# Performance work log

Hardware: AMD Instinct MI355X
Metric: run time of the kernel (lower is better)

The kernel has to match this reference:

```python
import jax, jax.numpy as jnp
import numpy as np
import math

LEVEL_SHAPES = [(100, 152), (50, 76), (25, 38), (13, 19)]
BS, E, NH, NL, NP = 2, 256, 8, 4, 4


def _grid_init_bias(num_heads, num_levels, num_points):
    # faithful to MultiScaleDeformableAttention.init_weights sampling_offsets bias
    thetas = jnp.arange(num_heads, dtype=jnp.float32) * (2.0 * math.pi / num_heads)
    grid = jnp.stack([jnp.cos(thetas), jnp.sin(thetas)], -1)  # [H,2]
    grid = grid / jnp.max(jnp.abs(grid), axis=-1, keepdims=True)
    grid = jnp.tile(grid[:, None, None, :], (1, num_levels, num_points, 1))  # [H,L,P,2]
    scale = jnp.arange(1, num_points + 1, dtype=jnp.float32)[None, None, :, None]
    return (grid * scale).reshape(-1)


def setup_inputs() -> dict:
    key = jax.random.key(0)
    ks = jax.random.split(key, 10)
    nv = sum(h * w for h, w in LEVEL_SHAPES)  # 20197
    nq = nv
    query = jax.random.normal(ks[0], (BS, nq, E), dtype=jnp.float32)
    value = jax.random.normal(ks[1], (BS, nv, E), dtype=jnp.float32)
    reference_points = jax.random.uniform(ks[2], (BS, nq, NL, 2), dtype=jnp.float32)
    spatial_shapes = jnp.array(LEVEL_SHAPES, dtype=jnp.int32)
    sizes = [h * w for h, w in LEVEL_SHAPES]
    level_start_index = jnp.array(np.cumsum([0] + sizes)[:-1], dtype=jnp.int32)
    s = 1.0 / math.sqrt(E)
    # Linear params stored as [in, out]; y = x @ W + b
    Wv = jax.random.normal(ks[3], (E, E), dtype=jnp.float32) * s
    bv = jnp.zeros((E,), jnp.float32)
    Wso = jax.random.normal(ks[4], (E, NH * NL * NP * 2), dtype=jnp.float32) * 0.01
    bso = _grid_init_bias(NH, NL, NP)
    Waw = jax.random.normal(ks[5], (E, NH * NL * NP), dtype=jnp.float32) * 0.01
    baw = jnp.zeros((NH * NL * NP,), jnp.float32)
    Wo = jax.random.normal(ks[6], (E, E), dtype=jnp.float32) * s
    bo = jnp.zeros((E,), jnp.float32)
    return dict(query=query, value=value, reference_points=reference_points,
                spatial_shapes=spatial_shapes, level_start_index=level_start_index,
                Wv=Wv, bv=bv, Wso=Wso, bso=bso, Waw=Waw, baw=baw, Wo=Wo, bo=bo)


def _bilinear_sample(vl, loc, h, w):
    # vl: [bs, nh, h*w, d]; loc: [bs, nq, nh, P, 2] normalized in [0,1]
    # matches F.grid_sample(mode='bilinear', padding_mode='zeros', align_corners=False)
    bs, nh, _, d = vl.shape
    nq, P = loc.shape[1], loc.shape[3]
    x = loc[..., 0] * w - 0.5
    y = loc[..., 1] * h - 0.5
    x0 = jnp.floor(x).astype(jnp.int32); x1 = x0 + 1
    y0 = jnp.floor(y).astype(jnp.int32); y1 = y0 + 1
    wx1 = x - x0; wx0 = 1.0 - wx1
    wy1 = y - y0; wy0 = 1.0 - wy1

    def gather(ix, iy):
        valid = ((ix >= 0) & (ix < w) & (iy >= 0) & (iy < h)).astype(vl.dtype)
        idx = jnp.clip(iy, 0, h - 1) * w + jnp.clip(ix, 0, w - 1)  # [bs,nq,nh,P]
        idx = jnp.transpose(idx, (0, 2, 1, 3)).reshape(bs, nh, nq * P)
        g = jnp.take_along_axis(vl, idx[..., None], axis=2)  # [bs,nh,nq*P,d]
        g = g.reshape(bs, nh, nq, P, d).transpose(0, 2, 1, 3, 4)  # [bs,nq,nh,P,d]
        return g * valid[..., None]

    return (gather(x0, y0) * (wx0 * wy0)[..., None]
            + gather(x1, y0) * (wx1 * wy0)[..., None]
            + gather(x0, y1) * (wx0 * wy1)[..., None]
            + gather(x1, y1) * (wx1 * wy1)[..., None])


def reference(query, value, reference_points, spatial_shapes, level_start_index,
              Wv, bv, Wso, bso, Waw, baw, Wo, bo):
    bs, nq, e = query.shape
    nv = value.shape[1]
    nh, nl, npt = NH, NL, NP
    d = e // nh
    shapes = np.asarray(spatial_shapes)          # static level shapes
    starts = np.asarray(level_start_index)

    v = (value @ Wv + bv).reshape(bs, nv, nh, d).transpose(0, 2, 1, 3)  # [bs,nh,nv,d]
    so = (query @ Wso + bso).reshape(bs, nq, nh, nl, npt, 2)
    aw = jax.nn.softmax((query @ Waw + baw).reshape(bs, nq, nh, nl * npt), axis=-1)
    aw = aw.reshape(bs, nq, nh, nl, npt)

    # offset normalizer is (w, h) per level
    offset_norm = jnp.stack([spatial_shapes[:, 1], spatial_shapes[:, 0]], -1).astype(query.dtype)
    loc = reference_points[:, :, None, :, None, :] + so / offset_norm[None, None, None, :, None, :]

    out = jnp.zeros((bs, nq, nh, d), dtype=query.dtype)
    for l in range(nl):
        h, w = int(shapes[l, 0]), int(shapes[l, 1])
        s = int(starts[l])
        vl = v[:, :, s:s + h * w, :]                      # [bs,nh,h*w,d]
        sampled = _bilinear_sample(vl, loc[:, :, :, l], h, w)  # [bs,nq,nh,P,d]
        out = out + jnp.einsum('bqhpd,bqhp->bqhd', sampled, aw[:, :, :, l])

    out = out.reshape(bs, nq, e) @ Wo + bo
    return out + query  # identity residual (dropout in eval mode)
```

## Files before the change

kernel.cpp:

```cpp
#include <hip/hip_runtime.h>
#include <hip/hip_bf16.h>
#include <math.h>

constexpr int kBS = 2;
constexpr int kNQ = 20197;
constexpr int kNV = 20197;
constexpr int kM  = kBS * kNQ;
constexpr int kMpad = 40448;

__constant__ int cLH[4] = {100, 50, 25, 13};
__constant__ int cLW[4] = {152, 76, 38, 19};
__constant__ int cLS[4] = {0, 15200, 19000, 19950};

typedef __bf16 bf16x8 __attribute__((ext_vector_type(8)));
typedef float  f32x4  __attribute__((ext_vector_type(4)));

__device__ __forceinline__ unsigned short f2bf(float x) {
    unsigned u = __float_as_uint(x);
    return (unsigned short)((u + 0x7fffu + ((u >> 16) & 1u)) >> 16);
}
__device__ __forceinline__ unsigned pack2(float a, float b) {
    return (unsigned)f2bf(a) | ((unsigned)f2bf(b) << 16);
}
__device__ __forceinline__ float bflo(unsigned u) { return __uint_as_float(u << 16); }
__device__ __forceinline__ float bfhi(unsigned u) { return __uint_as_float(u & 0xffff0000u); }
__device__ __forceinline__ void gload_lds16(const void* g, void* s) {
    __builtin_amdgcn_global_load_lds(
        (const __attribute__((address_space(1))) void*)g,
        (__attribute__((address_space(3))) void*)s, 16, 0, 0);
}

__global__ __launch_bounds__(256) void prep(
    const float* __restrict__ Wv, const float* __restrict__ Wso,
    const float* __restrict__ Waw, const float* __restrict__ Wo,
    const float* __restrict__ bso, const float* __restrict__ baw,
    unsigned short* __restrict__ WvT, unsigned short* __restrict__ WsoawT,
    unsigned short* __restrict__ WoT, float* __restrict__ bias384)
{
    int i = blockIdx.x * 256 + threadIdx.x;
    if (i < 65536) { int n = i >> 8, k = i & 255; WvT[i] = f2bf(Wv[k * 256 + n]); return; }
    i -= 65536;
    if (i < 98304) {
        int n = i >> 8, k = i & 255;
        WsoawT[i] = f2bf(n < 256 ? Wso[k * 256 + n] : Waw[k * 128 + (n - 256)]);
        return;
    }
    i -= 98304;
    if (i < 65536) { int n = i >> 8, k = i & 255; WoT[i] = f2bf(Wo[k * 256 + n]); return; }
    i -= 65536;
    if (i < 384) bias384[i] = (i < 256) ? bso[i] : baw[i - 256];
}

__global__ __launch_bounds__(256) void gemm_dual(
    const float* __restrict__ A0, const __hip_bfloat16* __restrict__ BT0,
    const float* __restrict__ bias0, unsigned short* __restrict__ C0,
    const float* __restrict__ A1, const __hip_bfloat16* __restrict__ BT1,
    const float* __restrict__ bias1, unsigned short* __restrict__ C1)
{
    constexpr int APITCH = 40;
    __shared__ __hip_bfloat16 As[128 * APITCH];
    __shared__ __hip_bfloat16 Bs[128 * 32];

    const int bx = blockIdx.x;
    const bool second = bx >= 2;
    const float* A = second ? A1 : A0;
    const __hip_bfloat16* BT = second ? BT1 : BT0;
    const float* bias = second ? bias1 : bias0;
    unsigned short* C = second ? C1 : C0;
    const int N = second ? 384 : 256;
    const int n0 = (second ? bx - 2 : bx) * 128;
    const int m0 = blockIdx.y * 128;

    const int t = threadIdx.x;
    const int wave = t >> 6, lane = t & 63;
    const int quad = lane >> 4, l16 = lane & 15;
    const int mw = (wave & 1) * 64, nw = (wave >> 1) * 64;
    const int sm = t >> 1;
    const int sh = (t & 1) * 16;

    f32x4 acc[4][4] = {};

    for (int k0 = 0; k0 < 256; k0 += 32) {
        __syncthreads();
        {
            const char* bt = (const char*)BT;
            #pragma unroll
            for (int j = 0; j < 2; ++j) {
                int off = j * 4096 + t * 16;
                int row = off >> 6, kb = off & 63;
                gload_lds16(bt + (size_t)(n0 + row) * 512 + k0 * 2 + kb,
                            (char*)Bs + off);
            }
        }
        {
            float4 f0 = make_float4(0.f, 0.f, 0.f, 0.f), f1 = f0, f2 = f0, f3 = f0;
            if (m0 + sm < kM) {
                const float4* p = (const float4*)(A + (size_t)(m0 + sm) * 256 + k0 + sh);
                f0 = p[0]; f1 = p[1]; f2 = p[2]; f3 = p[3];
            }
            uint4 q0 = make_uint4(pack2(f0.x, f0.y), pack2(f0.z, f0.w),
                                  pack2(f1.x, f1.y), pack2(f1.z, f1.w));
            uint4 q1 = make_uint4(pack2(f2.x, f2.y), pack2(f2.z, f2.w),
                                  pack2(f3.x, f3.y), pack2(f3.z, f3.w));
            uint4* dst = (uint4*)(void*)&As[sm * APITCH + sh];
            dst[0] = q0; dst[1] = q1;
        }
        __syncthreads();
        bf16x8 afr[4], bfr[4];
        #pragma unroll
        for (int mt = 0; mt < 4; ++mt)
            afr[mt] = *(const bf16x8*)(const void*)&As[(mw + mt * 16 + l16) * APITCH + quad * 8];
        #pragma unroll
        for (int nt = 0; nt < 4; ++nt)
            bfr[nt] = *(const bf16x8*)(const void*)&Bs[(nw + nt * 16 + l16) * 32 + quad * 8];
        #pragma unroll
        for (int mt = 0; mt < 4; ++mt)
            #pragma unroll
            for (int nt = 0; nt < 4; ++nt)
                acc[mt][nt] = __builtin_amdgcn_mfma_f32_16x16x32_bf16(
                    afr[mt], bfr[nt], acc[mt][nt], 0, 0, 0);
    }

    #pragma unroll
    for (int nt = 0; nt < 4; ++nt) {
        int col = n0 + nw + nt * 16 + l16;
        float bvv = bias[col];
        #pragma unroll
        for (int mt = 0; mt < 4; ++mt) {
            #pragma unroll
            for (int i = 0; i < 4; ++i) {
                int row = m0 + mw + mt * 16 + quad * 4 + i;
                if (row < kM)
                    C[(size_t)row * N + col] = f2bf(acc[mt][nt][i] + bvv);
            }
        }
    }
}

__global__ __launch_bounds__(256) void gemm_final(
    const __hip_bfloat16* __restrict__ Ab, const __hip_bfloat16* __restrict__ BT,
    const float* __restrict__ bias, const float* __restrict__ res,
    float* __restrict__ C)
{
    __shared__ __hip_bfloat16 As[128 * 32];
    __shared__ __hip_bfloat16 Bs[128 * 32];

    const int t = threadIdx.x;
    const int wave = t >> 6, lane = t & 63;
    const int quad = lane >> 4, l16 = lane & 15;
    const int mw = (wave & 1) * 64, nw = (wave >> 1) * 64;
    const int m0 = blockIdx.y * 128, n0 = blockIdx.x * 128;

    f32x4 acc[4][4] = {};

    for (int k0 = 0; k0 < 256; k0 += 32) {
        __syncthreads();
        const char* bt = (const char*)BT;
        const char* ab = (const char*)Ab;
        #pragma unroll
        for (int j = 0; j < 2; ++j) {
            int off = j * 4096 + t * 16;
            int row = off >> 6, kb = off & 63;
            gload_lds16(bt + (size_t)(n0 + row) * 512 + k0 * 2 + kb, (char*)Bs + off);
            gload_lds16(ab + (size_t)(m0 + row) * 512 + k0 * 2 + kb, (char*)As + off);
        }
        __syncthreads();
        bf16x8 afr[4], bfr[4];
        #pragma unroll
        for (int mt = 0; mt < 4; ++mt)
            afr[mt] = *(const bf16x8*)(const void*)&As[(mw + mt * 16 + l16) * 32 + quad * 8];
        #pragma unroll
        for (int nt = 0; nt < 4; ++nt)
            bfr[nt] = *(const bf16x8*)(const void*)&Bs[(nw + nt * 16 + l16) * 32 + quad * 8];
        #pragma unroll
        for (int mt = 0; mt < 4; ++mt)
            #pragma unroll
            for (int nt = 0; nt < 4; ++nt)
                acc[mt][nt] = __builtin_amdgcn_mfma_f32_16x16x32_bf16(
                    afr[mt], bfr[nt], acc[mt][nt], 0, 0, 0);
    }

    #pragma unroll
    for (int nt = 0; nt < 4; ++nt) {
        int col = n0 + nw + nt * 16 + l16;
        float bvv = bias[col];
        #pragma unroll
        for (int mt = 0; mt < 4; ++mt) {
            #pragma unroll
            for (int i = 0; i < 4; ++i) {
                int row = m0 + mw + mt * 16 + quad * 4 + i;
                if (row < kM)
                    C[(size_t)row * 256 + col] =
                        acc[mt][nt][i] + bvv + res[(size_t)row * 256 + col];
            }
        }
    }
}

__global__ __launch_bounds__(256) void msda_sample(
    const __hip_bfloat16* __restrict__ v,
    const __hip_bfloat16* __restrict__ soaw,
    const float* __restrict__ rp,
    __hip_bfloat16* __restrict__ mid)
{
    __shared__ int   sOff[512 * 4];
    __shared__ float sW[512 * 4];
    const int t = threadIdx.x;

    #pragma unroll
    for (int it = 0; it < 2; ++it) {
        const int idx = it * 256 + t;
        const int q = idx >> 7, r = idx & 127;
        const int h = r >> 4, lp = r & 15, l = lp >> 2;
        const int bq = blockIdx.x * 4 + q;
        const bool ok = bq < kM;

        unsigned sopk = 0; float logit = 0.f;
        float2 rr = make_float2(0.f, 0.f);
        if (ok) {
            sopk  = *(const unsigned*)(const void*)(soaw + (size_t)bq * 384 + 2 * r);
            logit = bflo((unsigned)*(const unsigned short*)(const void*)
                         (soaw + (size_t)bq * 384 + 256 + r));
            rr    = *(const float2*)(rp + (size_t)bq * 8 + l * 2);
        }
        float sx = bflo(sopk), sy = bfhi(sopk);

        float mx = logit;
        #pragma unroll
        for (int s = 8; s >= 1; s >>= 1) mx = fmaxf(mx, __shfl_xor(mx, s, 16));
        float e = __expf(logit - mx);
        float sum = e;
        #pragma unroll
        for (int s = 8; s >= 1; s >>= 1) sum += __shfl_xor(sum, s, 16);
        float w = e / sum;

        const int ww = cLW[l], hh = cLH[l];
        const float fw = (float)ww, fh = (float)hh;
        float x = rr.x * fw + sx - 0.5f;
        float y = rr.y * fh + sy - 0.5f;
        float xf = floorf(x), yf = floorf(y);
        int x0 = (int)xf, y0 = (int)yf;
        float wx1 = x - xf, wx0 = 1.f - wx1;
        float wy1 = y - yf, wy0 = 1.f - wy1;
        bool vx0 = (x0 >= 0) & (x0 < ww);
        bool vx1 = (x0 >= -1) & (x0 + 1 < ww);
        bool vy0 = (y0 >= 0) & (y0 < hh);
        bool vy1 = (y0 >= -1) & (y0 + 1 < hh);
        int cx0 = min(max(x0, 0), ww - 1);
        int cx1 = min(max(x0 + 1, 0), ww - 1);
        int cy0 = min(max(y0, 0), hh - 1);
        int cy1 = min(max(y0 + 1, 0), hh - 1);
        const int base = cLS[l] * 256 + h * 32;

        const int slot = q * 128 + lp * 8 + (h ^ (lp & 7));
        ((int4*)sOff)[slot] = make_int4(base + (cy0 * ww + cx0) * 256,
                                        base + (cy0 * ww + cx1) * 256,
                                        base + (cy1 * ww + cx0) * 256,
                                        base + (cy1 * ww + cx1) * 256);
        ((float4*)sW)[slot] = make_float4((vx0 & vy0) ? w * wx0 * wy0 : 0.f,
                                          (vx1 & vy0) ? w * wx1 * wy0 : 0.f,
                                          (vx0 & vy1) ? w * wx0 * wy1 : 0.f,
                                          (vx1 & vy1) ? w * wx1 * wy1 : 0.f);
    }
    __syncthreads();

    const int q = t >> 6, h = (t >> 3) & 7, c = (t & 7) * 4;
    const int bq = blockIdx.x * 4 + q;
    const int b = (bq >= kNQ) ? 1 : 0;
    const __hip_bfloat16* vb = v + (size_t)b * kNV * 256 + c;

    float a0 = 0.f, a1 = 0.f, a2 = 0.f, a3 = 0.f;
    #pragma unroll 4
    for (int pp = 0; pp < 16; ++pp) {
        const int slot = q * 128 + pp * 8 + (h ^ (pp & 7));
        int4   o = ((const int4*)sOff)[slot];
        float4 wv = ((const float4*)sW)[slot];
        {
            uint2 u = *(const uint2*)(const void*)(vb + o.x);
            a0 += wv.x * bflo(u.x); a1 += wv.x * bfhi(u.x);
            a2 += wv.x * bflo(u.y); a3 += wv.x * bfhi(u.y);
        }
        {
            uint2 u = *(const uint2*)(const void*)(vb + o.y);
            a0 += wv.y * bflo(u.x); a1 += wv.y * bfhi(u.x);
            a2 += wv.y * bflo(u.y); a3 += wv.y * bfhi(u.y);
        }
        {
            uint2 u = *(const uint2*)(const void*)(vb + o.z);
            a0 += wv.z * bflo(u.x); a1 += wv.z * bfhi(u.x);
            a2 += wv.z * bflo(u.y); a3 += wv.z * bfhi(u.y);
        }
        {
            uint2 u = *(const uint2*)(const void*)(vb + o.w);
            a0 += wv.w * bflo(u.x); a1 += wv.w * bfhi(u.x);
            a2 += wv.w * bflo(u.y); a3 += wv.w * bfhi(u.y);
        }
    }
    if (bq < kM) {
        uint2 pk = make_uint2(pack2(a0, a1), pack2(a2, a3));
        *(uint2*)(void*)(mid + (size_t)bq * 256 + h * 32 + c) = pk;
    }
}

extern "C" void kernel_launch(void* const* d_in, const int* in_sizes, int n_in,
                              void* d_out, int out_size, void* d_ws, size_t ws_size,
                              hipStream_t stream)
{
    const float* query = (const float*)d_in[0];
    const float* value = (const float*)d_in[1];
    const float* rp    = (const float*)d_in[2];
    const float* Wv  = (const float*)d_in[5];
    const float* bv  = (const float*)d_in[6];
    const float* Wso = (const float*)d_in[7];
    const float* bso = (const float*)d_in[8];
    const float* Waw = (const float*)d_in[9];
    const float* baw = (const float*)d_in[10];
    const float* Wo  = (const float*)d_in[11];
    const float* bo  = (const float*)d_in[12];

    __hip_bfloat16* v_b = (__hip_bfloat16*)d_out;

    char* ws8 = (char*)d_ws;
    __hip_bfloat16* soaw  = (__hip_bfloat16*)ws8;
    char* p = ws8 + (size_t)kM * 384 * 2;
    __hip_bfloat16* mid_b = (__hip_bfloat16*)p;  p += (size_t)kMpad * 256 * 2;
    unsigned short* WvT    = (unsigned short*)p; p += 256 * 256 * 2;
    unsigned short* WsoawT = (unsigned short*)p; p += 384 * 256 * 2;
    unsigned short* WoT    = (unsigned short*)p; p += 256 * 256 * 2;
    float* bias384         = (float*)p;

    hipLaunchKernelGGL(prep, dim3(898), dim3(256), 0, stream,
                       Wv, Wso, Waw, Wo, bso, baw, WvT, WsoawT, WoT, bias384);

    hipLaunchKernelGGL(gemm_dual, dim3(5, 316), dim3(256), 0, stream,
                       value, (const __hip_bfloat16*)WvT, bv, (unsigned short*)v_b,
                       query, (const __hip_bfloat16*)WsoawT, bias384, (unsigned short*)soaw);

    hipLaunchKernelGGL(msda_sample, dim3((kM + 3) / 4), dim3(256), 0, stream,
                       v_b, soaw, rp, mid_b);

    hipLaunchKernelGGL(gemm_final, dim3(2, 316), dim3(256), 0, stream,
                       mid_b, (const __hip_bfloat16*)WoT, bo, query, (float*)d_out);
}
```

Measured before the change: 339.9 us.

## Pre-convert activations to bf16, use async LDS loads for A, split sampling points across waves

The prep kernel becomes a grid-stride kernel that also converts value and query to bf16 up front. This lets the first GEMM load both A and B tiles straight into LDS with global_load_lds, instead of converting fp32 A in registers on every tile. The sampling kernel now handles two queries per block and splits each query's 16 points between two waves, combining the halves through shared memory. The padded shared layout is changed and the accumulation uses packed float2 math. In exchange there is an extra full read and write pass over value and query. Out-of-range row guards are also removed, and A rows beyond kM are read from the padded or adjacent buffer.

```diff
diff --git a/kernel.cpp b/kernel.cpp
--- a/kernel.cpp
+++ b/kernel.cpp
@@ -14,6 +14,7 @@
 
 typedef __bf16 bf16x8 __attribute__((ext_vector_type(8)));
 typedef float  f32x4  __attribute__((ext_vector_type(4)));
+typedef float  v2f    __attribute__((ext_vector_type(2)));
 
 __device__ __forceinline__ unsigned short f2bf(float x) {
     unsigned u = __float_as_uint(x);
@@ -30,44 +31,60 @@
         (__attribute__((address_space(3))) void*)s, 16, 0, 0);
 }
 
-__global__ __launch_bounds__(256) void prep(
+__global__ __launch_bounds__(256) void prep_all(
+    const float* __restrict__ value, const float* __restrict__ query,
     const float* __restrict__ Wv, const float* __restrict__ Wso,
     const float* __restrict__ Waw, const float* __restrict__ Wo,
     const float* __restrict__ bso, const float* __restrict__ baw,
+    unsigned short* __restrict__ value_b, unsigned short* __restrict__ query_b,
     unsigned short* __restrict__ WvT, unsigned short* __restrict__ WsoawT,
     unsigned short* __restrict__ WoT, float* __restrict__ bias384)
 {
-    int i = blockIdx.x * 256 + threadIdx.x;
-    if (i < 65536) { int n = i >> 8, k = i & 255; WvT[i] = f2bf(Wv[k * 256 + n]); return; }
-    i -= 65536;
-    if (i < 98304) {
-        int n = i >> 8, k = i & 255;
-        WsoawT[i] = f2bf(n < 256 ? Wso[k * 256 + n] : Waw[k * 128 + (n - 256)]);
-        return;
-    }
-    i -= 98304;
-    if (i < 65536) { int n = i >> 8, k = i & 255; WoT[i] = f2bf(Wo[k * 256 + n]); return; }
-    i -= 65536;
-    if (i < 384) bias384[i] = (i < 256) ? bso[i] : baw[i - 256];
+    constexpr int NC = kM * 256 / 8;
+    constexpr int NW = 65536 + 98304 + 65536 + 384;
+    const int stride = gridDim.x * 256;
+    for (int i = blockIdx.x * 256 + threadIdx.x; i < 2 * NC + NW; i += stride) {
+        if (i < 2 * NC) {
+            const bool isv = i < NC;
+            const int j = isv ? i : i - NC;
+            const float4* src = (const float4*)(isv ? value : query);
+            float4 f0 = src[2 * j], f1 = src[2 * j + 1];
+            uint4 q = make_uint4(pack2(f0.x, f0.y), pack2(f0.z, f0.w),
+                                 pack2(f1.x, f1.y), pack2(f1.z, f1.w));
+            ((uint4*)(isv ? value_b : query_b))[j] = q;
+        } else {
+            int k = i - 2 * NC;
+            if (k < 65536) { WvT[k] = f2bf(Wv[(k & 255) * 256 + (k >> 8)]); continue; }
+            k -= 65536;
+            if (k < 98304) {
+                int n = k >> 8, kk = k & 255;
+                WsoawT[k] = f2bf(n < 256 ? Wso[kk * 256 + n] : Waw[kk * 128 + (n - 256)]);
+                continue;
+            }
+            k -= 98304;
+            if (k < 65536) { WoT[k] = f2bf(Wo[(k & 255) * 256 + (k >> 8)]); continue; }
+            k -= 65536;
+            bias384[k] = (k < 256) ? bso[k] : baw[k - 256];
+        }
+    }
 }
 
 __global__ __launch_bounds__(256) void gemm_dual(
-    const float* __restrict__ A0, const __hip_bfloat16* __restrict__ BT0,
+    const __hip_bfloat16* __restrict__ A0, const __hip_bfloat16* __restrict__ BT0,
     const float* __restrict__ bias0, unsigned short* __restrict__ C0,
-    const float* __restrict__ A1, const __hip_bfloat16* __restrict__ BT1,
+    const __hip_bfloat16* __restrict__ A1, const __hip_bfloat16* __restrict__ BT1,
     const float* __restrict__ bias1, unsigned short* __restrict__ C1)
 {
-    constexpr int APITCH = 40;
-    __shared__ __hip_bfloat16 As[128 * APITCH];
+    __shared__ __hip_bfloat16 As[128 * 32];
     __shared__ __hip_bfloat16 Bs[128 * 32];
 
     const int bx = blockIdx.x;
     const bool second = bx >= 2;
-    const float* A = second ? A1 : A0;
+    const __hip_bfloat16* A  = second ? A1 : A0;
     const __hip_bfloat16* BT = second ? BT1 : BT0;
     const float* bias = second ? bias1 : bias0;
     unsigned short* C = second ? C1 : C0;
-    const int N = second ? 384 : 256;
+    const int N  = second ? 384 : 256;
     const int n0 = (second ? bx - 2 : bx) * 128;
     const int m0 = blockIdx.y * 128;
 
@@ -75,41 +92,25 @@
     const int wave = t >> 6, lane = t & 63;
     const int quad = lane >> 4, l16 = lane & 15;
     const int mw = (wave & 1) * 64, nw = (wave >> 1) * 64;
-    const int sm = t >> 1;
-    const int sh = (t & 1) * 16;
 
     f32x4 acc[4][4] = {};
 
     for (int k0 = 0; k0 < 256; k0 += 32) {
         __syncthreads();
-        {
-            const char* bt = (const char*)BT;
-            #pragma unroll
-            for (int j = 0; j < 2; ++j) {
-                int off = j * 4096 + t * 16;
-                int row = off >> 6, kb = off & 63;
-                gload_lds16(bt + (size_t)(n0 + row) * 512 + k0 * 2 + kb,
-                            (char*)Bs + off);
-            }
-        }
-        {
-            float4 f0 = make_float4(0.f, 0.f, 0.f, 0.f), f1 = f0, f2 = f0, f3 = f0;
-            if (m0 + sm < kM) {
-                const float4* p = (const float4*)(A + (size_t)(m0 + sm) * 256 + k0 + sh);
-                f0 = p[0]; f1 = p[1]; f2 = p[2]; f3 = p[3];
-            }
-            uint4 q0 = make_uint4(pack2(f0.x, f0.y), pack2(f0.z, f0.w),
-                                  pack2(f1.x, f1.y), pack2(f1.z, f1.w));
-            uint4 q1 = make_uint4(pack2(f2.x, f2.y), pack2(f2.z, f2.w),
-                                  pack2(f3.x, f3.y), pack2(f3.z, f3.w));
-            uint4* dst = (uint4*)(void*)&As[sm * APITCH + sh];
-            dst[0] = q0; dst[1] = q1;
+        const char* bt = (const char*)BT;
+        const char* ab = (const char*)A;
+        #pragma unroll
+        for (int j = 0; j < 2; ++j) {
+            int off = j * 4096 + t * 16;
+            int row = off >> 6, kb = off & 63;
+            gload_lds16(bt + (size_t)(n0 + row) * 512 + k0 * 2 + kb, (char*)Bs + off);
+            gload_lds16(ab + (size_t)(m0 + row) * 512 + k0 * 2 + kb, (char*)As + off);
         }
         __syncthreads();
         bf16x8 afr[4], bfr[4];
         #pragma unroll
         for (int mt = 0; mt < 4; ++mt)
-            afr[mt] = *(const bf16x8*)(const void*)&As[(mw + mt * 16 + l16) * APITCH + quad * 8];
+            afr[mt] = *(const bf16x8*)(const void*)&As[(mw + mt * 16 + l16) * 32 + quad * 8];
         #pragma unroll
         for (int nt = 0; nt < 4; ++nt)
             bfr[nt] = *(const bf16x8*)(const void*)&Bs[(nw + nt * 16 + l16) * 32 + quad * 8];
@@ -203,26 +204,19 @@
     const float* __restrict__ rp,
     __hip_bfloat16* __restrict__ mid)
 {
-    __shared__ int   sOff[512 * 4];
-    __shared__ float sW[512 * 4];
+    __shared__ int4   sOff[2 * 136];
+    __shared__ float4 sW[2 * 136];
+    __shared__ float4 sRed[128];
     const int t = threadIdx.x;
 
-    #pragma unroll
-    for (int it = 0; it < 2; ++it) {
-        const int idx = it * 256 + t;
-        const int q = idx >> 7, r = idx & 127;
+    {
+        const int q = t >> 7, r = t & 127;
         const int h = r >> 4, lp = r & 15, l = lp >> 2;
-        const int bq = blockIdx.x * 4 + q;
-        const bool ok = bq < kM;
-
-        unsigned sopk = 0; float logit = 0.f;
-        float2 rr = make_float2(0.f, 0.f);
-        if (ok) {
-            sopk  = *(const unsigned*)(const void*)(soaw + (size_t)bq * 384 + 2 * r);
-            logit = bflo((unsigned)*(const unsigned short*)(const void*)
-                         (soaw + (size_t)bq * 384 + 256 + r));
-            rr    = *(const float2*)(rp + (size_t)bq * 8 + l * 2);
-        }
+        const int bq = blockIdx.x * 2 + q;
+        unsigned sopk = *(const unsigned*)(const void*)(soaw + (size_t)bq * 384 + 2 * r);
+        float logit = bflo((unsigned)*(const unsigned short*)(const void*)
+                           (soaw + (size_t)bq * 384 + 256 + r));
+        float2 rr = *(const float2*)(rp + (size_t)bq * 8 + l * 2);
         float sx = bflo(sopk), sy = bfhi(sopk);
 
         float mx = logit;
@@ -252,52 +246,59 @@
         int cy1 = min(max(y0 + 1, 0), hh - 1);
         const int base = cLS[l] * 256 + h * 32;
 
-        const int slot = q * 128 + lp * 8 + (h ^ (lp & 7));
-        ((int4*)sOff)[slot] = make_int4(base + (cy0 * ww + cx0) * 256,
-                                        base + (cy0 * ww + cx1) * 256,
-                                        base + (cy1 * ww + cx0) * 256,
-                                        base + (cy1 * ww + cx1) * 256);
-        ((float4*)sW)[slot] = make_float4((vx0 & vy0) ? w * wx0 * wy0 : 0.f,
-                                          (vx1 & vy0) ? w * wx1 * wy0 : 0.f,
-                                          (vx0 & vy1) ? w * wx0 * wy1 : 0.f,
-                                          (vx1 & vy1) ? w * wx1 * wy1 : 0.f);
+        const int slot = q * 136 + h * 17 + lp;
+        sOff[slot] = make_int4(base + (cy0 * ww + cx0) * 256,
+                               base + (cy0 * ww + cx1) * 256,
+                               base + (cy1 * ww + cx0) * 256,
+                               base + (cy1 * ww + cx1) * 256);
+        sW[slot] = make_float4((vx0 & vy0) ? w * wx0 * wy0 : 0.f,
+                               (vx1 & vy0) ? w * wx1 * wy0 : 0.f,
+                               (vx0 & vy1) ? w * wx0 * wy1 : 0.f,
+                               (vx1 & vy1) ? w * wx1 * wy1 : 0.f);
     }
     __syncthreads();
 
-    const int q = t >> 6, h = (t >> 3) & 7, c = (t & 7) * 4;
-    const int bq = blockIdx.x * 4 + q;
+    const int wave = t >> 6, q = wave >> 1, half = wave & 1;
+    const int h = (t >> 3) & 7, c = (t & 7) * 4;
+    const int bq = blockIdx.x * 2 + q;
     const int b = (bq >= kNQ) ? 1 : 0;
     const __hip_bfloat16* vb = v + (size_t)b * kNV * 256 + c;
 
-    float a0 = 0.f, a1 = 0.f, a2 = 0.f, a3 = 0.f;
+    v2f acc01 = {0.f, 0.f}, acc23 = {0.f, 0.f};
     #pragma unroll 4
-    for (int pp = 0; pp < 16; ++pp) {
-        const int slot = q * 128 + pp * 8 + (h ^ (pp & 7));
-        int4   o = ((const int4*)sOff)[slot];
-        float4 wv = ((const float4*)sW)[slot];
+    for (int pp = 0; pp < 8; ++pp) {
+        const int slot = q * 136 + h * 17 + half * 8 + pp;
+        int4   o  = sOff[slot];
+        float4 wv = sW[slot];
         {
             uint2 u = *(const uint2*)(const void*)(vb + o.x);
-            a0 += wv.x * bflo(u.x); a1 += wv.x * bfhi(u.x);
-            a2 += wv.x * bflo(u.y); a3 += wv.x * bfhi(u.y);
+            v2f lo = {bflo(u.x), bfhi(u.x)}, hi = {bflo(u.y), bfhi(u.y)};
+            acc01 += wv.x * lo; acc23 += wv.x * hi;
         }
         {
             uint2 u = *(const uint2*)(const void*)(vb + o.y);
-            a0 += wv.y * bflo(u.x); a1 += wv.y * bfhi(u.x);
-            a2 += wv.y * bflo(u.y); a3 += wv.y * bfhi(u.y);
+            v2f lo = {bflo(u.x), bfhi(u.x)}, hi = {bflo(u.y), bfhi(u.y)};
+            acc01 += wv.y * lo; acc23 += wv.y * hi;
         }
         {
             uint2 u = *(const uint2*)(const void*)(vb + o.z);
-            a0 += wv.z * bflo(u.x); a1 += wv.z * bfhi(u.x);
-            a2 += wv.z * bflo(u.y); a3 += wv.z * bfhi(u.y);
+            v2f lo = {bflo(u.x), bfhi(u.x)}, hi = {bflo(u.y), bfhi(u.y)};
+            acc01 += wv.z * lo; acc23 += wv.z * hi;
         }
         {
             uint2 u = *(const uint2*)(const void*)(vb + o.w);
-            a0 += wv.w * bflo(u.x); a1 += wv.w * bfhi(u.x);
-            a2 += wv.w * bflo(u.y); a3 += wv.w * bfhi(u.y);
-        }
-    }
-    if (bq < kM) {
-        uint2 pk = make_uint2(pack2(a0, a1), pack2(a2, a3));
+            v2f lo = {bflo(u.x), bfhi(u.x)}, hi = {bflo(u.y), bfhi(u.y)};
+            acc01 += wv.w * lo; acc23 += wv.w * hi;
+        }
+    }
+
+    if (half)
+        sRed[q * 64 + (t & 63)] = make_float4(acc01.x, acc01.y, acc23.x, acc23.y);
+    __syncthreads();
+    if (!half) {
+        float4 o = sRed[q * 64 + (t & 63)];
+        uint2 pk = make_uint2(pack2(acc01.x + o.x, acc01.y + o.y),
+                              pack2(acc23.x + o.z, acc23.y + o.w));
         *(uint2*)(void*)(mid + (size_t)bq * 256 + h * 32 + c) = pk;
     }
 }
@@ -318,25 +319,29 @@
     const float* Wo  = (const float*)d_in[11];
     const float* bo  = (const float*)d_in[12];
 
-    __hip_bfloat16* v_b = (__hip_bfloat16*)d_out;
-
-    char* ws8 = (char*)d_ws;
-    __hip_bfloat16* soaw  = (__hip_bfloat16*)ws8;
-    char* p = ws8 + (size_t)kM * 384 * 2;
-    __hip_bfloat16* mid_b = (__hip_bfloat16*)p;  p += (size_t)kMpad * 256 * 2;
+    unsigned short* value_b = (unsigned short*)d_out;
+    __hip_bfloat16* v_b     = (__hip_bfloat16*)((char*)d_out + (size_t)kM * 512);
+
+    char* p = (char*)d_ws;
+    __hip_bfloat16* soaw = (__hip_bfloat16*)p;   p += (size_t)kM * 384 * 2;
+    unsigned short* query_b = (unsigned short*)p;
+    __hip_bfloat16* mid_b   = (__hip_bfloat16*)p; p += (size_t)kMpad * 256 * 2;
     unsigned short* WvT    = (unsigned short*)p; p += 256 * 256 * 2;
     unsigned short* WsoawT = (unsigned short*)p; p += 384 * 256 * 2;
     unsigned short* WoT    = (unsigned short*)p; p += 256 * 256 * 2;
     float* bias384         = (float*)p;
 
-    hipLaunchKernelGGL(prep, dim3(898), dim3(256), 0, stream,
-                       Wv, Wso, Waw, Wo, bso, baw, WvT, WsoawT, WoT, bias384);
+    hipLaunchKernelGGL(prep_all, dim3(2048), dim3(256), 0, stream,
+                       value, query, Wv, Wso, Waw, Wo, bso, baw,
+                       value_b, query_b, WvT, WsoawT, WoT, bias384);
 
     hipLaunchKernelGGL(gemm_dual, dim3(5, 316), dim3(256), 0, stream,
-                       value, (const __hip_bfloat16*)WvT, bv, (unsigned short*)v_b,
-                       query, (const __hip_bfloat16*)WsoawT, bias384, (unsigned short*)soaw);
-
-    hipLaunchKernelGGL(msda_sample, dim3((kM + 3) / 4), dim3(256), 0, stream,
+                       (const __hip_bfloat16*)value_b, (const __hip_bfloat16*)WvT,
+                       bv, (unsigned short*)v_b,
+                       (const __hip_bfloat16*)query_b, (const __hip_bfloat16*)WsoawT,
+                       bias384, (unsigned short*)soaw);
+
+    hipLaunchKernelGGL(msda_sample, dim3(kM / 2), dim3(256), 0, stream,
                        v_b, soaw, rp, mid_b);
 
     hipLaunchKernelGGL(gemm_final, dim3(2, 316), dim3(256), 0, stream,
```

Result: slower. 349.1 us (+2.7%).
